# Performance work log

Hardware: AMD Instinct MI355X
Metric: run time of the kernel (lower is better)

Reference implementation:

```python
import jax, jax.numpy as jnp
import numpy as np

ANG = 7
N = ANG * ANG          # 49 views
CENTER = N // 2        # index 24 = central view
EDGE_C = 150.0
ALPHA = 0.1
CROP = 8
GAUSS = jnp.array([[0.0751, 0.1238, 0.0751],
                   [0.1238, 0.2042, 0.1238],
                   [0.0751, 0.1238, 0.0751]], dtype=jnp.float32)


def _edge_aware_smoothness(D, I):
    # D: [b,h,w] disparity; I: [b,3,h,w] center view
    gx = I[:, :, :, 1:] - I[:, :, :, :-1]
    gy = I[:, :, 1:, :] - I[:, :, :-1, :]
    wx = jnp.exp(-EDGE_C * jnp.mean(jnp.abs(gx), axis=1, keepdims=True))
    wy = jnp.exp(-EDGE_C * jnp.mean(jnp.abs(gy), axis=1, keepdims=True))
    Du = D[:, None]
    dgx = Du[:, :, :, 1:] - Du[:, :, :, :-1]
    dgy = Du[:, :, 1:, :] - Du[:, :, :-1, :]
    lx = jnp.mean((wx * jnp.abs(dgx))[:, :, CROP:-CROP, CROP:-CROP])
    ly = jnp.mean((wy * jnp.abs(dgy))[:, :, CROP:-CROP, CROP:-CROP])
    return (lx + ly) / 2.0


def _warp_all(pred, x):
    # Backward-warp each of the 49 views toward the center view using the
    # per-pixel disparity scaled by the view's angular offset (bilinear,
    # border-clamped) -- standard light-field warping (warp_all in the repo).
    # pred: [b,h,w]; x: [b,3,N,h,w] -> warped [b,3,N,h,w]
    b, c, n, h, w = x.shape
    off = jnp.arange(ANG, dtype=pred.dtype) - (ANG // 2)
    du = jnp.repeat(off, ANG)   # row (u) offset per view, [N]
    dv = jnp.tile(off, ANG)     # col (v) offset per view, [N]
    gy = jnp.arange(h, dtype=pred.dtype)[:, None]
    gx = jnp.arange(w, dtype=pred.dtype)[None, :]
    p = pred[:, None, :, :]                                # [b,1,h,w]
    cy = jnp.clip(gy[None, None] + p * du[None, :, None, None], 0.0, h - 1)
    cx = jnp.clip(gx[None, None] + p * dv[None, :, None, None], 0.0, w - 1)
    y0f = jnp.floor(cy); x0f = jnp.floor(cx)
    ty = (cy - y0f)[..., None]; tx = (cx - x0f)[..., None]
    y0 = y0f.astype(jnp.int32); x0 = x0f.astype(jnp.int32)
    y1 = jnp.minimum(y0 + 1, h - 1); x1 = jnp.minimum(x0 + 1, w - 1)
    img = jnp.transpose(x, (0, 2, 3, 4, 1)).reshape(b, n, h * w, c)

    def gather(yi, xi):
        idx = (yi * w + xi).reshape(b, n, h * w, 1)
        return jnp.take_along_axis(img, idx, axis=2).reshape(b, n, h, w, c)

    out = (gather(y0, x0) * (1 - ty) * (1 - tx)
           + gather(y0, x1) * (1 - ty) * tx
           + gather(y1, x0) * ty * (1 - tx)
           + gather(y1, x1) * ty * tx)
    return jnp.transpose(out, (0, 4, 1, 2, 3))


def _gauss_smooth_angular(cl):
    # cl [b,1,N,h,w]: 3x3 gaussian conv over the 7x7 angular grid, replicate pad
    b, _, _, h, w = cl.shape
    g = cl.reshape(b, 1, ANG, ANG, h, w)
    g = jnp.pad(g, ((0, 0), (0, 0), (1, 1), (1, 1), (0, 0), (0, 0)), mode='edge')
    out = sum(GAUSS[i, j] * g[:, :, i:i + ANG, j:j + ANG]
              for i in range(3) for j in range(3))
    return out.reshape(b, 1, N, h, w)


def _forward(pred, x, y, epoch):
    b, u, v, h, w, c = x.shape
    # 'b u v h w c -> b c (u v) h w'
    xr = jnp.transpose(x, (0, 5, 1, 2, 3, 4)).reshape(b, c, N, h, w)
    center = xr[:, :, CENTER]                               # [b,3,h,w]
    grad_loss = _edge_aware_smoothness(pred, center)
    warped = _warp_all(pred, xr)                            # [b,3,N,h,w]
    color_loss = jnp.mean(jnp.abs(warped - warped[:, :, CENTER:CENTER + 1]),
                          axis=1, keepdims=True)            # [b,1,N,h,w]
    if epoch > 0:
        gauss = jax.lax.stop_gradient(_gauss_smooth_angular(color_loss))
        idx = jnp.argsort(-gauss, axis=2)                   # descending
        sorted_cl = jnp.take_along_axis(color_loss, idx, axis=2)
    else:
        sorted_cl = -jnp.sort(-color_loss, axis=2)
    yb = y[:, None, None, :, :]
    ar = jnp.arange(N, dtype=y.dtype)[None, None, :, None, None]
    mask = (ar > yb).astype(color_loss.dtype) / (N - yb) * N
    if epoch > 0:
        mask = jax.lax.stop_gradient(mask)                  # torch no_grad branch
    cl = jnp.mean((sorted_cl * mask)[..., CROP:-CROP, CROP:-CROP])
    return cl + grad_loss * ALPHA


def setup_inputs():
    key = jax.random.key(0)
    k1, k2, k3 = jax.random.split(key, 3)
    b, h, w = 4, 256, 256
    pred = jax.random.normal(k1, (b, h, w), dtype=jnp.float32)
    x = jax.random.uniform(k2, (b, ANG, ANG, h, w, 3), dtype=jnp.float32)
    y = jax.random.uniform(k3, (b, h, w), dtype=jnp.float32) * 24.0  # keep ~half views
    return {"pred": pred, "x": x, "y": y, "epoch": 5}


def reference(pred, x, y, epoch):
    return _forward(pred, x, y, epoch)
```

## Files before the change

kernel.cpp:

```cpp
#include <hip/hip_runtime.h>
#include <math.h>

#define NV    49
#define Himg  256
#define Wimg  256
#define RW    240
#define RWH   (RW*RW)
#define NPIX  (4*RWH)
#define ROWF  (Wimg*3)
#define IMGF  (Himg*Wimg*3)
#define NBLK  (NPIX/64)

typedef float f4u __attribute__((ext_vector_type(4), aligned(4)));
typedef float f2u __attribute__((ext_vector_type(2), aligned(4)));


__global__ __launch_bounds__(448, 4) void color_kernel(
    const float* __restrict__ pred, const float* __restrict__ x,
    const float* __restrict__ y, const int* __restrict__ epoch_p,
    double* __restrict__ acc)
{
    __shared__ float s_cl[64 * NV];
    __shared__ float s_g [64 * NV];
    __shared__ float sred[8];

    const int tid = threadIdx.x;
    const int pix = tid & 63;
    const int sub = __builtin_amdgcn_readfirstlane(tid >> 6);

    int lb  = (blockIdx.x & 7) * (NBLK/8) + (blockIdx.x >> 3);
    int pid = lb * 64 + pix;
    int b   = pid / RWH;
    int rem = pid - b * RWH;
    int ry  = rem / RW;
    int yy  = 8 + ry;
    int xx  = 8 + (rem - ry * RW);

    int pidx = (b * Himg + yy) * Wimg + xx;
    float p = pred[pidx];
    const int epoch = *epoch_p;

    const float* xv    = x + (size_t)b * (49 * IMGF);
    const float* cbase = xv + (24 * IMGF) + (yy * Wimg + xx) * 3;
    f4u cv = *(const f4u*)cbase;
    float c0 = cv.x, c1 = cv.y, c2 = cv.z;

    float* mycl = s_cl + pix * NV;
    float* myg  = s_g  + pix * NV;

    int co[7]; float txv[7];
    #pragma unroll
    for (int vv = 0; vv < 7; vv++) {
        float cx = fminf(fmaxf((float)xx + p * (float)(vv-3), 0.0f), 255.0f);
        float x0f = floorf(cx);
        float tx = cx - x0f;
        int ix0 = (int)x0f;
        if (ix0 >= 255) { ix0 = 254; tx = 1.0f; }
        co[vv] = ix0 * 3; txv[vv] = tx;
    }

    float creg[7];
    {
        float cy = fminf(fmaxf((float)yy + p * (float)(sub-3), 0.0f), 255.0f);
        float y0f = floorf(cy);
        float ty = cy - y0f;
        int iy0 = (int)y0f;
        int iy1 = min(iy0+1, 255);
        int ro0 = iy0*ROWF, ro1 = iy1*ROWF;
        const float* vbase = xv + sub * 7 * IMGF;

        f4u a0[7], b0[7]; f2u a1[7], b1[7];
        #pragma unroll
        for (int vv = 0; vv < 7; vv++) {
            const float* s0p = vbase + vv*IMGF + ro0 + co[vv];
            const float* s1p = vbase + vv*IMGF + ro1 + co[vv];
            a0[vv] = *(const f4u*)s0p;
            a1[vv] = *(const f2u*)(s0p + 4);
            b0[vv] = *(const f4u*)s1p;
            b1[vv] = *(const f2u*)(s1p + 4);
        }

        #pragma unroll
        for (int vv = 0; vv < 7; vv++) {
            float tx = txv[vv];
            float s00 = a0[vv].x, s01 = a0[vv].y, s02 = a0[vv].z;
            float s03 = a0[vv].w, s04 = a1[vv].x, s05 = a1[vv].y;
            float s10 = b0[vv].x, s11 = b0[vv].y, s12 = b0[vv].z;
            float s13 = b0[vv].w, s14 = b1[vv].x, s15 = b1[vv].y;
            float h0 = s00 + tx*(s03-s00);
            float h1 = s01 + tx*(s04-s01);
            float h2 = s02 + tx*(s05-s02);
            float k0 = s10 + tx*(s13-s10);
            float k1 = s11 + tx*(s14-s11);
            float k2 = s12 + tx*(s15-s12);
            float o0 = h0 + ty*(k0-h0);
            float o1 = h1 + ty*(k1-h1);
            float o2 = h2 + ty*(k2-h2);
            float cl = (fabsf(o0-c0)+fabsf(o1-c1)+fabsf(o2-c2)) * (1.0f/3.0f);
            creg[vv] = cl;
            mycl[sub*7 + vv] = cl;
        }
    }

    if (sub == 3) {
        float lx = 0.0f, ly = 0.0f;
        if (xx <= 246) {
            f4u q0 = *(const f4u*)cbase;
            f2u q1 = *(const f2u*)(cbase + 4);
            float wx = __expf(-50.0f * (fabsf(q0.w-c0) + fabsf(q1.x-c1) + fabsf(q1.y-c2)));
            lx = wx * fabsf(pred[pidx + 1] - p);
        }
        if (yy <= 246) {
            f4u r = *(const f4u*)(cbase + ROWF);
            float wy = __expf(-50.0f * (fabsf(r.x-c0) + fabsf(r.y-c1) + fabsf(r.z-c2)));
            ly = wy * fabsf(pred[pidx + Wimg] - p);
        }
        #pragma unroll
        for (int off = 32; off > 0; off >>= 1) {
            lx += __shfl_down(lx, off);
            ly += __shfl_down(ly, off);
        }
        if (pix == 0) {
            atomicAdd(acc + 1, (double)lx);
            atomicAdd(acc + 2, (double)ly);
        }
    }
    __syncthreads();

    if (epoch > 0) {
        const int um1 = (sub > 0) ? sub-1 : 0;
        const int up1 = (sub < 6) ? sub+1 : 6;
        const float* rm = mycl + um1*7;
        const float* rc = mycl + sub*7;
        const float* rp = mycl + up1*7;
        #pragma unroll
        for (int vv = 0; vv < 7; vv++) {
            const int vm = (vv > 0) ? vv-1 : 0;
            const int vp = (vv < 6) ? vv+1 : 6;
            myg[sub*7 + vv] =
                0.0751f*rm[vm] + 0.1238f*rm[vv] + 0.0751f*rm[vp] +
                0.1238f*rc[vm] + 0.2042f*rc[vv] + 0.1238f*rc[vp] +
                0.0751f*rp[vm] + 0.1238f*rp[vv] + 0.0751f*rp[vp];
        }
    }
    __syncthreads();

    const float* key = (epoch > 0) ? myg : mycl;
    float yval = y[pidx];

    unsigned long long kn[7];
    int cnt[7];
    #pragma unroll
    for (int i = 0; i < 7; i++) {
        int n = sub*7 + i;
        unsigned int bb = __float_as_uint(key[n]);
        kn[i] = (((unsigned long long)bb) << 8) | (unsigned long long)(255 - n);
        cnt[i] = 0;
    }
    #pragma unroll 7
    for (int m = 0; m < NV; m++) {
        unsigned int bm = __float_as_uint(key[m]);
        unsigned long long km = (((unsigned long long)bm) << 8) | (unsigned long long)(255 - m);
        #pragma unroll
        for (int i = 0; i < 7; i++)
            cnt[i] += (km > kn[i]) ? 1 : 0;
    }
    float tail = 0.0f;
    #pragma unroll
    for (int i = 0; i < 7; i++)
        tail += ((float)cnt[i] > yval) ? creg[i] : 0.0f;
    float contrib = tail * (49.0f / (49.0f - yval));

    #pragma unroll
    for (int off = 32; off > 0; off >>= 1)
        contrib += __shfl_down(contrib, off);
    if (pix == 0) sred[sub] = contrib;
    __syncthreads();
    if (tid == 0) {
        double s = 0.0;
        #pragma unroll
        for (int i = 0; i < 7; i++) s += (double)sred[i];
        atomicAdd(acc + 0, s);
    }
}

__global__ void finalize_kernel(const double* __restrict__ acc,
                                float* __restrict__ out)
{
    double cl = acc[0] / 11289600.0;
    double gl = (acc[1] + acc[2]) / (2.0 * 229440.0);
    out[0] = (float)(cl + 0.1 * gl);
}

extern "C" void kernel_launch(void* const* d_in, const int* in_sizes, int n_in,
                              void* d_out, int out_size, void* d_ws, size_t ws_size,
                              hipStream_t stream)
{
    const float* pred  = (const float*)d_in[0];
    const float* x     = (const float*)d_in[1];
    const float* y     = (const float*)d_in[2];
    const int*   epoch = (const int*)d_in[3];
    double* acc = (double*)d_ws;

    hipMemsetAsync(acc, 0, 3 * sizeof(double), stream);
    color_kernel<<<NBLK, 448, 0, stream>>>(pred, x, y, epoch, acc);
    finalize_kernel<<<1, 1, 0, stream>>>(acc, (float*)d_out);
}
```

Before: 339.8 us.

## Software-pipeline view gathers and vectorize LDS key reads with padded rows

Replaces the load-all-then-compute loop over seven views with a rotating four-slot prefetch. Loads run three views ahead of the bilinear math, with sched_barriers to hold that order, which lowers register pressure while keeping gathers in flight. The per-pixel LDS rows are padded from 49 to 52 floats so the rank-sort keys can be read as 13 aligned float4 loads instead of 49 scalar loads, and the compare loop is fully unrolled. Risks are the scheduling barriers limiting the compiler's freedom, the larger unroll costing registers, and a change in LDS bank patterns from the stride of 52.

```diff
diff --git a/kernel.cpp b/kernel.cpp
--- a/kernel.cpp
+++ b/kernel.cpp
@@ -2,6 +2,7 @@
 #include <math.h>
 
 #define NV    49
+#define NVP   52
 #define Himg  256
 #define Wimg  256
 #define RW    240
@@ -13,6 +14,7 @@
 
 typedef float f4u __attribute__((ext_vector_type(4), aligned(4)));
 typedef float f2u __attribute__((ext_vector_type(2), aligned(4)));
+typedef float f4a __attribute__((ext_vector_type(4), aligned(16)));
 
 
 __global__ __launch_bounds__(448, 4) void color_kernel(
@@ -20,8 +22,8 @@
     const float* __restrict__ y, const int* __restrict__ epoch_p,
     double* __restrict__ acc)
 {
-    __shared__ float s_cl[64 * NV];
-    __shared__ float s_g [64 * NV];
+    __shared__ float s_cl[64 * NVP];
+    __shared__ float s_g [64 * NVP];
     __shared__ float sred[8];
 
     const int tid = threadIdx.x;
@@ -37,7 +39,8 @@
     int xx  = 8 + (rem - ry * RW);
 
     int pidx = (b * Himg + yy) * Wimg + xx;
-    float p = pred[pidx];
+    float p    = pred[pidx];
+    float yval = y[pidx];
     const int epoch = *epoch_p;
 
     const float* xv    = x + (size_t)b * (49 * IMGF);
@@ -45,8 +48,8 @@
     f4u cv = *(const f4u*)cbase;
     float c0 = cv.x, c1 = cv.y, c2 = cv.z;
 
-    float* mycl = s_cl + pix * NV;
-    float* myg  = s_g  + pix * NV;
+    float* mycl = s_cl + pix * NVP;
+    float* myg  = s_g  + pix * NVP;
 
     int co[7]; float txv[7];
     #pragma unroll
@@ -69,24 +72,27 @@
         int ro0 = iy0*ROWF, ro1 = iy1*ROWF;
         const float* vbase = xv + sub * 7 * IMGF;
 
-        f4u a0[7], b0[7]; f2u a1[7], b1[7];
+        f4u a0[4], b0[4]; f2u a1[4], b1[4];
+
+#define LOADV(VV, S) { \
+        const float* s0p = vbase + (VV)*IMGF + ro0 + co[VV]; \
+        const float* s1p = vbase + (VV)*IMGF + ro1 + co[VV]; \
+        a0[S] = *(const f4u*)s0p;  a1[S] = *(const f2u*)(s0p + 4); \
+        b0[S] = *(const f4u*)s1p;  b1[S] = *(const f2u*)(s1p + 4); }
+
+        LOADV(0,0) LOADV(1,1) LOADV(2,2)
+        __builtin_amdgcn_sched_barrier(0);
+
         #pragma unroll
         for (int vv = 0; vv < 7; vv++) {
-            const float* s0p = vbase + vv*IMGF + ro0 + co[vv];
-            const float* s1p = vbase + vv*IMGF + ro1 + co[vv];
-            a0[vv] = *(const f4u*)s0p;
-            a1[vv] = *(const f2u*)(s0p + 4);
-            b0[vv] = *(const f4u*)s1p;
-            b1[vv] = *(const f2u*)(s1p + 4);
-        }
-
-        #pragma unroll
-        for (int vv = 0; vv < 7; vv++) {
+            if (vv + 3 < 7) { LOADV(vv+3, (vv+3)&3) }
+            __builtin_amdgcn_sched_barrier(0);
+            const int S = vv & 3;
             float tx = txv[vv];
-            float s00 = a0[vv].x, s01 = a0[vv].y, s02 = a0[vv].z;
-            float s03 = a0[vv].w, s04 = a1[vv].x, s05 = a1[vv].y;
-            float s10 = b0[vv].x, s11 = b0[vv].y, s12 = b0[vv].z;
-            float s13 = b0[vv].w, s14 = b1[vv].x, s15 = b1[vv].y;
+            float s00 = a0[S].x, s01 = a0[S].y, s02 = a0[S].z;
+            float s03 = a0[S].w, s04 = a1[S].x, s05 = a1[S].y;
+            float s10 = b0[S].x, s11 = b0[S].y, s12 = b0[S].z;
+            float s13 = b0[S].w, s14 = b1[S].x, s15 = b1[S].y;
             float h0 = s00 + tx*(s03-s00);
             float h1 = s01 + tx*(s04-s01);
             float h2 = s02 + tx*(s05-s02);
@@ -99,7 +105,9 @@
             float cl = (fabsf(o0-c0)+fabsf(o1-c1)+fabsf(o2-c2)) * (1.0f/3.0f);
             creg[vv] = cl;
             mycl[sub*7 + vv] = cl;
-        }
+            __builtin_amdgcn_sched_barrier(0);
+        }
+#undef LOADV
     }
 
     if (sub == 3) {
@@ -145,21 +153,25 @@
     }
     __syncthreads();
 
-    const float* key = (epoch > 0) ? myg : mycl;
-    float yval = y[pidx];
+    const float* keyb = (epoch > 0) ? myg : mycl;
+
+    f4a kv[13];
+    #pragma unroll
+    for (int i = 0; i < 13; i++)
+        kv[i] = *(const f4a*)(keyb + 4*i);
 
     unsigned long long kn[7];
     int cnt[7];
     #pragma unroll
     for (int i = 0; i < 7; i++) {
         int n = sub*7 + i;
-        unsigned int bb = __float_as_uint(key[n]);
+        unsigned int bb = __float_as_uint(keyb[n]);
         kn[i] = (((unsigned long long)bb) << 8) | (unsigned long long)(255 - n);
         cnt[i] = 0;
     }
-    #pragma unroll 7
+    #pragma unroll
     for (int m = 0; m < NV; m++) {
-        unsigned int bm = __float_as_uint(key[m]);
+        unsigned int bm = __float_as_uint(kv[m>>2][m&3]);
         unsigned long long km = (((unsigned long long)bm) << 8) | (unsigned long long)(255 - m);
         #pragma unroll
         for (int i = 0; i < 7; i++)
```

New measurement: 320.3 us. 1.06x faster.
